# Kernel tuning notes

Measured on AMD Instinct MI355X. Metric: run time of the kernel, lower is better.

## Reference

```python
import jax, jax.numpy as jnp
import numpy as np

B, S, HID = 4, 2048, 1024
H, DH = 16, 64  # HID = H * DH
ADP, NTASKS = 64, 10
GATE_S = 100.0  # s (soft gate temperature), != smax=400 so no hard threshold


def setup_inputs() -> dict:
    key = jax.random.key(0)
    ks = jax.random.split(key, 13)
    sc = 0.02
    return {
        "hidden_states": jax.random.normal(ks[0], (B, S, HID), jnp.float32),
        "Wq": jax.random.normal(ks[1], (HID, HID), jnp.float32) * sc,
        "bq": jax.random.normal(ks[2], (HID,), jnp.float32) * sc,
        "Wk": jax.random.normal(ks[3], (HID, HID), jnp.float32) * sc,
        "bk": jax.random.normal(ks[4], (HID,), jnp.float32) * sc,
        "Wv": jax.random.normal(ks[5], (HID, HID), jnp.float32) * sc,
        "bv": jax.random.normal(ks[6], (HID,), jnp.float32) * sc,
        "fc1_w": jax.random.normal(ks[7], (HID, ADP), jnp.float32) * sc,
        "fc1_b": jax.random.normal(ks[8], (ADP,), jnp.float32) * sc,
        "fc2_w": jax.random.normal(ks[9], (ADP, HID), jnp.float32) * sc,
        "fc2_b": jax.random.normal(ks[10], (HID,), jnp.float32) * sc,
        "efc1": jax.random.normal(ks[11], (NTASKS, ADP), jnp.float32),
        "efc2": jax.random.normal(ks[12], (NTASKS, HID), jnp.float32),
        "t": 3,
    }


def reference(hidden_states, Wq, bq, Wk, bk, Wv, bv,
              fc1_w, fc1_b, fc2_w, fc2_b, efc1, efc2, t):
    x = hidden_states
    # --- parallel adapter with task gates (add_residual=False) ---
    gfc1 = jax.nn.sigmoid(GATE_S * efc1[t])  # [ADP]
    gfc2 = jax.nn.sigmoid(GATE_S * efc2[t])  # [HID]
    h = jax.nn.relu(x @ fc1_w + fc1_b) * gfc1          # [B,S,ADP]
    adapter_out = jax.nn.relu(h @ fc2_w + fc2_b) * gfc2  # [B,S,HID]
    # --- multi-head self-attention (absolute positions, no mask, eval dropout) ---
    def split_heads(y):  # [B,S,HID] -> [B,H,S,DH]
        return y.reshape(B, S, H, DH).transpose(0, 2, 1, 3)
    q = split_heads(x @ Wq + bq)
    k = split_heads(x @ Wk + bk)
    v = split_heads(x @ Wv + bv)
    scores = jnp.einsum("bhqd,bhkd->bhqk", q, k) / np.sqrt(DH).astype(jnp.float32)
    probs = jax.nn.softmax(scores, axis=-1)
    ctx = jnp.einsum("bhqk,bhkd->bhqd", probs, v)
    ctx = ctx.transpose(0, 2, 1, 3).reshape(B, S, HID)
    return ctx + adapter_out
```

## Files before the change

kernel.cpp:

```cpp
#include <hip/hip_runtime.h>
#include <stdint.h>
#include <stddef.h>

typedef unsigned short u16;
typedef unsigned int u32;
typedef __bf16 bf16x8 __attribute__((ext_vector_type(8)));
typedef short s16x4 __attribute__((ext_vector_type(4)));
typedef float f32x4 __attribute__((ext_vector_type(4)));

#define BB  4
#define SS  2048
#define HIDD 1024
#define NH  16
#define DHD 64

#define GLD16(gaddr, laddr) \
  __builtin_amdgcn_global_load_lds( \
      (const __attribute__((address_space(1))) u32*)(gaddr), \
      (__attribute__((address_space(3))) u32*)(laddr), 16, 0, 0)

#define LDS_BARRIER() asm volatile("s_waitcnt lgkmcnt(0)\n\ts_barrier" ::: "memory")

__device__ __forceinline__ u16 f2b(float f){
  union { float f; unsigned u; } c; c.f = f;
  unsigned r = c.u + 0x7fffu + ((c.u >> 16) & 1u);
  return (u16)(r >> 16);
}
__device__ __forceinline__ u16 f2b_fast(float f){
  union { float f; unsigned u; } c; c.f = f;
  return (u16)((c.u + 0x8000u) >> 16);
}
__device__ __forceinline__ f32x4 mfma32(bf16x8 a, bf16x8 b, f32x4 c){
  return __builtin_amdgcn_mfma_f32_16x16x32_bf16(a, b, c, 0, 0, 0);
}
__device__ __forceinline__ f32x4 mfma16(s16x4 a, s16x4 b, f32x4 c){
  return __builtin_amdgcn_mfma_f32_16x16x16bf16_1k(a, b, c, 0, 0, 0);
}

__global__ __launch_bounds__(256)
void prep(const float* __restrict__ x, u16* __restrict__ xb,
          const float* __restrict__ Wq, const float* __restrict__ Wk,
          const float* __restrict__ Wv, const float* __restrict__ f1w,
          const float* __restrict__ f2w,
          u16* __restrict__ wqkv, u16* __restrict__ wtf1, u16* __restrict__ wtf2)
{
  __shared__ float tile[32][33];
  int blk = blockIdx.x;
  const int tid = threadIdx.x;
  if (blk < 8192) {
    int i = blk * 1024 + tid * 4;
    float4 v = *reinterpret_cast<const float4*>(&x[i]);
    ushort4 o;
    o.x = f2b(v.x); o.y = f2b(v.y); o.z = f2b(v.z); o.w = f2b(v.w);
    *reinterpret_cast<ushort4*>(&xb[i]) = o;
    return;
  }
  blk -= 8192;
  const float* in; u16* out; int R, C, c0, r0;
  if (blk < 3072) {
    int m = blk >> 10, t = blk & 1023;
    in = (m == 0) ? Wq : (m == 1) ? Wk : Wv;
    out = wqkv + (size_t)m * 1024 * 1024;
    R = 1024; C = 1024; c0 = (t & 31) * 32; r0 = (t >> 5) * 32;
  } else if (blk < 3136) {
    int t = blk - 3072;
    in = f1w; out = wtf1; R = 1024; C = 64;
    c0 = (t & 1) * 32; r0 = (t >> 1) * 32;
  } else {
    int t = blk - 3136;
    in = f2w; out = wtf2; R = 64; C = 1024;
    c0 = (t & 31) * 32; r0 = (t >> 5) * 32;
  }
  int tx = tid & 31, ty = tid >> 5;
  #pragma unroll
  for (int j = 0; j < 32; j += 8)
    tile[ty + j][tx] = in[(size_t)(r0 + ty + j) * C + c0 + tx];
  __syncthreads();
  #pragma unroll
  for (int j = 0; j < 32; j += 8)
    out[(size_t)(c0 + ty + j) * R + r0 + tx] = f2b(tile[tx][ty + j]);
}

__global__ __launch_bounds__(256)
void gemm_qkv(const u16* __restrict__ X, const u16* __restrict__ Wt,
              const float* __restrict__ bq, const float* __restrict__ bk,
              const float* __restrict__ bv,
              u16* __restrict__ qb, u16* __restrict__ kb, u16* __restrict__ vt)
{
  constexpr int K = 1024;
  __shared__ __align__(16) u16 ldsX[128 * 32];
  __shared__ __align__(16) u16 ldsW[128 * 32];
  const int tid = threadIdx.x;
  const int w = tid >> 6, lane = tid & 63, quad = lane >> 4, ln = lane & 15;
  const int m0 = blockIdx.y * 128, n0 = blockIdx.x * 128;
  const int wrow = (w >> 1) * 64;
  const int wcol = (w & 1) * 64;
  const int srow = tid >> 2;
  const int scol = (tid & 3) * 8;

  f32x4 acc[4][4] = {};

  for (int k0 = 0; k0 < K; k0 += 32) {
    #pragma unroll
    for (int c = 0; c < 2; ++c)
      GLD16(&X[(size_t)(m0 + c * 64 + srow) * K + k0 + scol], &ldsX[c * 2048 + w * 512]);
    #pragma unroll
    for (int c = 0; c < 2; ++c)
      GLD16(&Wt[(size_t)(n0 + c * 64 + srow) * K + k0 + scol], &ldsW[c * 2048 + w * 512]);
    __syncthreads();

    bf16x8 a[4], bfr[4];
    #pragma unroll
    for (int mt = 0; mt < 4; ++mt)
      a[mt] = *reinterpret_cast<const bf16x8*>(&ldsX[(wrow + mt * 16 + ln) * 32 + quad * 8]);
    #pragma unroll
    for (int nt = 0; nt < 4; ++nt)
      bfr[nt] = *reinterpret_cast<const bf16x8*>(&ldsW[(wcol + nt * 16 + ln) * 32 + quad * 8]);
    #pragma unroll
    for (int mt = 0; mt < 4; ++mt)
      #pragma unroll
      for (int nt = 0; nt < 4; ++nt)
        acc[mt][nt] = mfma32(a[mt], bfr[nt], acc[mt][nt]);
    __syncthreads();
  }

  if (n0 < 2048) {
    const float scale = (n0 < 1024) ? 0.125f : 1.f;
    const float* bias = (n0 < 1024) ? bq : bk;
    u16* dst = (n0 < 1024) ? qb : kb;
    const int nb = n0 & 1023;
    #pragma unroll
    for (int nt = 0; nt < 4; ++nt) {
      const int col = nb + wcol + nt * 16 + ln;
      const float bvv = bias[col];
      #pragma unroll
      for (int mt = 0; mt < 4; ++mt)
        #pragma unroll
        for (int r = 0; r < 4; ++r) {
          int row = m0 + wrow + mt * 16 + quad * 4 + r;
          dst[(size_t)row * 1024 + col] = f2b((acc[mt][nt][r] + bvv) * scale);
        }
    }
  } else {
    #pragma unroll
    for (int nt = 0; nt < 4; ++nt) {
      const int colv = (n0 - 2048) + wcol + nt * 16 + ln;
      const float bvv = bv[colv];
      const int h = colv >> 6, d = colv & 63;
      #pragma unroll
      for (int mt = 0; mt < 4; ++mt) {
        int row = m0 + wrow + mt * 16 + quad * 4;
        int bb = row >> 11, s = row & 2047;
        ushort4 o;
        o.x = f2b(acc[mt][nt][0] + bvv);
        o.y = f2b(acc[mt][nt][1] + bvv);
        o.z = f2b(acc[mt][nt][2] + bvv);
        o.w = f2b(acc[mt][nt][3] + bvv);
        *reinterpret_cast<ushort4*>(
            &vt[((((size_t)bb * NH + h) * DHD + d) << 11) + s]) = o;
      }
    }
  }
}

template<int BM, int BN, int WR, int WC>
__global__ __launch_bounds__(256)
void gemm_bt(const u16* __restrict__ X, const u16* __restrict__ Wt,
             const float* __restrict__ bias, void* __restrict__ outv,
             int M, int N, int K, int mode,
             const float* __restrict__ gate, const int* __restrict__ tptr)
{
  constexpr int MT = BM / (WR * 16);
  constexpr int NT = BN / (WC * 16);
  __shared__ __align__(16) u16 ldsX[BM * 32];
  __shared__ __align__(16) u16 ldsW[BN * 32];
  const int tid = threadIdx.x;
  const int w = tid >> 6, lane = tid & 63, quad = lane >> 4, ln = lane & 15;
  const int m0 = blockIdx.y * BM, n0 = blockIdx.x * BN;
  const int wrow = (w / WC) * (MT * 16);
  const int wcol = (w % WC) * (NT * 16);
  const int srow = tid >> 2;
  const int scol = (tid & 3) * 8;

  f32x4 acc[MT][NT] = {};

  for (int k0 = 0; k0 < K; k0 += 32) {
    #pragma unroll
    for (int c = 0; c < BM / 64; ++c)
      GLD16(&X[(size_t)(m0 + c * 64 + srow) * K + k0 + scol], &ldsX[c * 2048 + w * 512]);
    #pragma unroll
    for (int c = 0; c < BN / 64; ++c)
      GLD16(&Wt[(size_t)(n0 + c * 64 + srow) * K + k0 + scol], &ldsW[c * 2048 + w * 512]);
    __syncthreads();

    bf16x8 a[MT], bfr[NT];
    #pragma unroll
    for (int mt = 0; mt < MT; ++mt)
      a[mt] = *reinterpret_cast<const bf16x8*>(&ldsX[(wrow + mt * 16 + ln) * 32 + quad * 8]);
    #pragma unroll
    for (int nt = 0; nt < NT; ++nt)
      bfr[nt] = *reinterpret_cast<const bf16x8*>(&ldsW[(wcol + nt * 16 + ln) * 32 + quad * 8]);
    #pragma unroll
    for (int mt = 0; mt < MT; ++mt)
      #pragma unroll
      for (int nt = 0; nt < NT; ++nt)
        acc[mt][nt] = mfma32(a[mt], bfr[nt], acc[mt][nt]);
    __syncthreads();
  }

  int t = tptr[0];
  if ((unsigned)t > 9u) t = 0;
  #pragma unroll
  for (int nt = 0; nt < NT; ++nt) {
    const int col = n0 + wcol + nt * 16 + ln;
    const float bvv = bias[col];
    const float g = 1.f / (1.f + __expf(-100.f * gate[t * N + col]));
    #pragma unroll
    for (int mt = 0; mt < MT; ++mt) {
      #pragma unroll
      for (int r = 0; r < 4; ++r) {
        int row = m0 + wrow + mt * 16 + quad * 4 + r;
        float v = fmaxf(acc[mt][nt][r] + bvv, 0.f) * g;
        if (mode == 2) ((float*)outv)[(size_t)row * N + col] = v;
        else           ((u16*)outv)[(size_t)row * N + col] = f2b(v);
      }
    }
  }
}

__global__ __launch_bounds__(256, 4)
void attn(const u16* __restrict__ Q, const u16* __restrict__ Kb,
          const u16* __restrict__ Vt, const float* adap, float* out)
{
  __shared__ __align__(16) u16 ldsK[64 * 72];
  __shared__ __align__(16) u16 ldsV[64 * 72];

  const int tid = threadIdx.x;
  const int w = tid >> 6, lane = tid & 63, quad = lane >> 4, ln = lane & 15;
  const int h = blockIdx.x, b = blockIdx.y, qt = blockIdx.z;
  const int bh = b * NH + h;
  const int qbase = qt * 128 + w * 32;
  const int skey = tid >> 3;
  const int sd   = (tid & 7) * 8;

  bf16x8 qf[2][2];
  #pragma unroll
  for (int q2 = 0; q2 < 2; ++q2)
    #pragma unroll
    for (int kk = 0; kk < 2; ++kk)
      qf[q2][kk] = *reinterpret_cast<const bf16x8*>(
          &Q[(size_t)(b * SS + qbase + q2 * 16 + ln) * HIDD + h * DHD + kk * 32 + quad * 8]);

  f32x4 o[4][2] = {};
  float lsum[2] = {0.f, 0.f};

  const u16* Kp = &Kb[(size_t)(b * SS + skey) * HIDD + h * DHD + sd];
  const u16* Vp = &Vt[((size_t)bh * DHD + skey) * SS + sd];

  uint4 rK0 = *reinterpret_cast<const uint4*>(Kp);
  uint4 rK1 = *reinterpret_cast<const uint4*>(Kp + (size_t)32 * HIDD);
  uint4 rV0 = *reinterpret_cast<const uint4*>(Vp);
  uint4 rV1 = *reinterpret_cast<const uint4*>(Vp + (size_t)32 * SS);

  for (int kt = 0; kt < SS; kt += 64) {
    LDS_BARRIER();
    *reinterpret_cast<uint4*>(&ldsK[skey * 72 + sd])        = rK0;
    *reinterpret_cast<uint4*>(&ldsK[(32 + skey) * 72 + sd]) = rK1;
    *reinterpret_cast<uint4*>(&ldsV[skey * 72 + sd])        = rV0;
    *reinterpret_cast<uint4*>(&ldsV[(32 + skey) * 72 + sd]) = rV1;
    if (kt + 64 < SS) {
      const u16* Kn = Kp + (size_t)(kt + 64) * HIDD;
      const u16* Vn = Vp + (kt + 64);
      rK0 = *reinterpret_cast<const uint4*>(Kn);
      rK1 = *reinterpret_cast<const uint4*>(Kn + (size_t)32 * HIDD);
      rV0 = *reinterpret_cast<const uint4*>(Vn);
      rV1 = *reinterpret_cast<const uint4*>(Vn + (size_t)32 * SS);
    }
    LDS_BARRIER();

    f32x4 s[4][2];
    #pragma unroll
    for (int k4 = 0; k4 < 4; ++k4) {
      bf16x8 kf0 = *reinterpret_cast<const bf16x8*>(&ldsK[(k4 * 16 + ln) * 72 + quad * 8]);
      bf16x8 kf1 = *reinterpret_cast<const bf16x8*>(&ldsK[(k4 * 16 + ln) * 72 + 32 + quad * 8]);
      #pragma unroll
      for (int q2 = 0; q2 < 2; ++q2) {
        f32x4 z = {0.f, 0.f, 0.f, 0.f};
        z = mfma32(kf0, qf[q2][0], z);
        z = mfma32(kf1, qf[q2][1], z);
        s[k4][q2] = z;
      }
    }

    s16x4 p[4][2];
    #pragma unroll
    for (int k4 = 0; k4 < 4; ++k4)
      #pragma unroll
      for (int q2 = 0; q2 < 2; ++q2)
        #pragma unroll
        for (int r = 0; r < 4; ++r) {
          float pv = __expf(s[k4][q2][r]);
          lsum[q2] += pv;
          p[k4][q2][r] = (short)f2b_fast(pv);
        }

    #pragma unroll
    for (int dt = 0; dt < 4; ++dt) {
      #pragma unroll
      for (int ks = 0; ks < 4; ++ks) {
        s16x4 vf = *reinterpret_cast<const s16x4*>(
            &ldsV[(dt * 16 + ln) * 72 + ks * 16 + quad * 4]);
        #pragma unroll
        for (int q2 = 0; q2 < 2; ++q2)
          o[dt][q2] = mfma16(vf, p[ks][q2], o[dt][q2]);
      }
    }
  }

  float rl[2];
  #pragma unroll
  for (int q2 = 0; q2 < 2; ++q2) {
    float v = lsum[q2];
    v += __shfl_xor(v, 16);
    v += __shfl_xor(v, 32);
    rl[q2] = 1.f / v;
  }

  #pragma unroll
  for (int q2 = 0; q2 < 2; ++q2) {
    const int q = qbase + q2 * 16 + ln;
    float* orow = &out[(size_t)(b * SS + q) * HIDD + h * DHD];
    const float* arow = &adap[(size_t)(b * SS + q) * HIDD + h * DHD];
    #pragma unroll
    for (int dt = 0; dt < 4; ++dt)
      #pragma unroll
      for (int r = 0; r < 4; ++r) {
        int d = dt * 16 + quad * 4 + r;
        orow[d] = o[dt][q2][r] * rl[q2] + arow[d];
      }
  }
}

extern "C" void kernel_launch(void* const* d_in, const int* in_sizes, int n_in,
                              void* d_out, int out_size, void* d_ws, size_t ws_size,
                              hipStream_t stream) {
  const float* x    = (const float*)d_in[0];
  const float* Wq   = (const float*)d_in[1];
  const float* bq   = (const float*)d_in[2];
  const float* Wk   = (const float*)d_in[3];
  const float* bk   = (const float*)d_in[4];
  const float* Wv   = (const float*)d_in[5];
  const float* bv   = (const float*)d_in[6];
  const float* f1w  = (const float*)d_in[7];
  const float* f1b  = (const float*)d_in[8];
  const float* f2w  = (const float*)d_in[9];
  const float* f2b_ = (const float*)d_in[10];
  const float* efc1 = (const float*)d_in[11];
  const float* efc2 = (const float*)d_in[12];
  const int*   tptr = (const int*)d_in[13];
  float* out = (float*)d_out;

  unsigned char* ws = (unsigned char*)d_ws;
  u16* xb   = (u16*)(ws + 0);
  u16* wqkv = (u16*)(ws + (16u << 20));
  u16* wtf1 = (u16*)(ws + (22u << 20));
  u16* wtf2 = (u16*)(ws + (22u << 20) + (128u << 10));
  u16* hb   = (u16*)(ws + (23u << 20));
  u16* qb   = (u16*)(ws + (24u << 20));
  u16* kb   = (u16*)(ws + (40u << 20));
  u16* vt   = (u16*)(ws + (56u << 20));

  prep<<<dim3(11392), 256, 0, stream>>>(x, xb, Wq, Wk, Wv, f1w, f2w,
                                        wqkv, wtf1, wtf2);

  gemm_qkv<<<dim3(24, 64), 256, 0, stream>>>(xb, wqkv, bq, bk, bv, qb, kb, vt);

  gemm_bt<64,64,2,2><<<dim3(1, 128), 256, 0, stream>>>(
      xb, wtf1, f1b, hb, 8192, 64, 1024, 1, efc1, tptr);
  gemm_bt<128,128,2,2><<<dim3(8, 64), 256, 0, stream>>>(
      hb, wtf2, f2b_, out, 8192, 1024, 64, 2, efc2, tptr);

  attn<<<dim3(NH, BB, SS / 128), 256, 0, stream>>>(qb, kb, vt, out, out);
}
```

Measured before the change: 310.8 us.

## Fuse adapter fc2 GEMM into attention epilogue and use exp2 softmax

Removes the separate fc2 GEMM launch that wrote a full fp32 adapter tensor to the output, which attention then read back. Instead, each attention block computes its 64-column slice of relu(h@fc2_w+b)*gate with MFMAs in the epilogue. The separate fc2 launch and an fp32 write plus read of the full output go away, at the cost of extra MFMA work and loads of hb and w2 per attention block. The change also folds log2(e) into the Q scale so softmax can use the hardware exp2, and pads the V LDS row stride to 76 to change the bank-conflict pattern.

```diff
diff --git a/kernel.cpp b/kernel.cpp
--- a/kernel.cpp
+++ b/kernel.cpp
@@ -20,6 +20,12 @@
       (__attribute__((address_space(3))) u32*)(laddr), 16, 0, 0)
 
 #define LDS_BARRIER() asm volatile("s_waitcnt lgkmcnt(0)\n\ts_barrier" ::: "memory")
+
+#if __has_builtin(__builtin_amdgcn_exp2f)
+  #define EXP2(x) __builtin_amdgcn_exp2f(x)
+#else
+  #define EXP2(x) __expf((x) * 0.6931471805599453f)
+#endif
 
 __device__ __forceinline__ u16 f2b(float f){
   union { float f; unsigned u; } c; c.f = f;
@@ -125,7 +131,7 @@
   }
 
   if (n0 < 2048) {
-    const float scale = (n0 < 1024) ? 0.125f : 1.f;
+    const float scale = (n0 < 1024) ? 0.18033688f : 1.f;
     const float* bias = (n0 < 1024) ? bq : bk;
     u16* dst = (n0 < 1024) ? qb : kb;
     const int nb = n0 & 1023;
@@ -166,8 +172,8 @@
 template<int BM, int BN, int WR, int WC>
 __global__ __launch_bounds__(256)
 void gemm_bt(const u16* __restrict__ X, const u16* __restrict__ Wt,
-             const float* __restrict__ bias, void* __restrict__ outv,
-             int M, int N, int K, int mode,
+             const float* __restrict__ bias, u16* __restrict__ outp,
+             int M, int N, int K,
              const float* __restrict__ gate, const int* __restrict__ tptr)
 {
   constexpr int MT = BM / (WR * 16);
@@ -220,9 +226,7 @@
       #pragma unroll
       for (int r = 0; r < 4; ++r) {
         int row = m0 + wrow + mt * 16 + quad * 4 + r;
-        float v = fmaxf(acc[mt][nt][r] + bvv, 0.f) * g;
-        if (mode == 2) ((float*)outv)[(size_t)row * N + col] = v;
-        else           ((u16*)outv)[(size_t)row * N + col] = f2b(v);
+        outp[(size_t)row * N + col] = f2b(fmaxf(acc[mt][nt][r] + bvv, 0.f) * g);
       }
     }
   }
@@ -230,10 +234,13 @@
 
 __global__ __launch_bounds__(256, 4)
 void attn(const u16* __restrict__ Q, const u16* __restrict__ Kb,
-          const u16* __restrict__ Vt, const float* adap, float* out)
+          const u16* __restrict__ Vt, const u16* __restrict__ hb,
+          const u16* __restrict__ w2, const float* __restrict__ b2,
+          const float* __restrict__ gate2, const int* __restrict__ tptr,
+          float* __restrict__ out)
 {
   __shared__ __align__(16) u16 ldsK[64 * 72];
-  __shared__ __align__(16) u16 ldsV[64 * 72];
+  __shared__ __align__(16) u16 ldsV[64 * 76];
 
   const int tid = threadIdx.x;
   const int w = tid >> 6, lane = tid & 63, quad = lane >> 4, ln = lane & 15;
@@ -266,8 +273,8 @@
     LDS_BARRIER();
     *reinterpret_cast<uint4*>(&ldsK[skey * 72 + sd])        = rK0;
     *reinterpret_cast<uint4*>(&ldsK[(32 + skey) * 72 + sd]) = rK1;
-    *reinterpret_cast<uint4*>(&ldsV[skey * 72 + sd])        = rV0;
-    *reinterpret_cast<uint4*>(&ldsV[(32 + skey) * 72 + sd]) = rV1;
+    *reinterpret_cast<uint4*>(&ldsV[skey * 76 + sd])        = rV0;
+    *reinterpret_cast<uint4*>(&ldsV[(32 + skey) * 76 + sd]) = rV1;
     if (kt + 64 < SS) {
       const u16* Kn = Kp + (size_t)(kt + 64) * HIDD;
       const u16* Vn = Vp + (kt + 64);
@@ -299,7 +306,7 @@
       for (int q2 = 0; q2 < 2; ++q2)
         #pragma unroll
         for (int r = 0; r < 4; ++r) {
-          float pv = __expf(s[k4][q2][r]);
+          float pv = EXP2(s[k4][q2][r]);
           lsum[q2] += pv;
           p[k4][q2][r] = (short)f2b_fast(pv);
         }
@@ -309,7 +316,7 @@
       #pragma unroll
       for (int ks = 0; ks < 4; ++ks) {
         s16x4 vf = *reinterpret_cast<const s16x4*>(
-            &ldsV[(dt * 16 + ln) * 72 + ks * 16 + quad * 4]);
+            &ldsV[(dt * 16 + ln) * 76 + ks * 16 + quad * 4]);
         #pragma unroll
         for (int q2 = 0; q2 < 2; ++q2)
           o[dt][q2] = mfma16(vf, p[ks][q2], o[dt][q2]);
@@ -326,17 +333,49 @@
     rl[q2] = 1.f / v;
   }
 
+  f32x4 acc2[4][2] = {};
+  #pragma unroll
+  for (int kk = 0; kk < 2; ++kk) {
+    bf16x8 hf[2];
+    #pragma unroll
+    for (int q2 = 0; q2 < 2; ++q2) {
+      int q = qbase + q2 * 16 + ln;
+      hf[q2] = *reinterpret_cast<const bf16x8*>(
+          &hb[(size_t)(b * SS + q) * 64 + kk * 32 + quad * 8]);
+    }
+    #pragma unroll
+    for (int dt = 0; dt < 4; ++dt) {
+      bf16x8 wf = *reinterpret_cast<const bf16x8*>(
+          &w2[(size_t)(h * DHD + dt * 16 + ln) * 64 + kk * 32 + quad * 8]);
+      #pragma unroll
+      for (int q2 = 0; q2 < 2; ++q2)
+        acc2[dt][q2] = mfma32(wf, hf[q2], acc2[dt][q2]);
+    }
+  }
+
+  int t = tptr[0];
+  if ((unsigned)t > 9u) t = 0;
+  float bv2[4][4], gv2[4][4];
+  #pragma unroll
+  for (int dt = 0; dt < 4; ++dt)
+    #pragma unroll
+    for (int r = 0; r < 4; ++r) {
+      int col = h * DHD + dt * 16 + quad * 4 + r;
+      bv2[dt][r] = b2[col];
+      gv2[dt][r] = 1.f / (1.f + __expf(-100.f * gate2[t * HIDD + col]));
+    }
+
   #pragma unroll
   for (int q2 = 0; q2 < 2; ++q2) {
     const int q = qbase + q2 * 16 + ln;
     float* orow = &out[(size_t)(b * SS + q) * HIDD + h * DHD];
-    const float* arow = &adap[(size_t)(b * SS + q) * HIDD + h * DHD];
     #pragma unroll
     for (int dt = 0; dt < 4; ++dt)
       #pragma unroll
       for (int r = 0; r < 4; ++r) {
         int d = dt * 16 + quad * 4 + r;
-        orow[d] = o[dt][q2][r] * rl[q2] + arow[d];
+        float ad = fmaxf(acc2[dt][q2][r] + bv2[dt][r], 0.f) * gv2[dt][r];
+        orow[d] = o[dt][q2][r] * rl[q2] + ad;
       }
   }
 }
@@ -376,9 +415,8 @@
   gemm_qkv<<<dim3(24, 64), 256, 0, stream>>>(xb, wqkv, bq, bk, bv, qb, kb, vt);
 
   gemm_bt<64,64,2,2><<<dim3(1, 128), 256, 0, stream>>>(
-      xb, wtf1, f1b, hb, 8192, 64, 1024, 1, efc1, tptr);
-  gemm_bt<128,128,2,2><<<dim3(8, 64), 256, 0, stream>>>(
-      hb, wtf2, f2b_, out, 8192, 1024, 64, 2, efc2, tptr);
-
-  attn<<<dim3(NH, BB, SS / 128), 256, 0, stream>>>(qb, kb, vt, out, out);
-}
+      xb, wtf1, f1b, hb, 8192, 64, 1024, efc1, tptr);
+
+  attn<<<dim3(NH, BB, SS / 128), 256, 0, stream>>>(
+      qb, kb, vt, hb, wtf2, f2b_, efc2, tptr, out);
+}
```

Result: faster. 291.6 us (-6.2%).
